# Optimization experiments

Hardware: AMD Instinct MI355X
Metric: run time of the kernel (lower is better)

Reference implementation:

```python
import jax, jax.numpy as jnp
import numpy as np

N_NODES = 50000
N_EDGES = 1600000
IN_DIM = 128
HIDDEN = 16
HEADS = 8
OUT_DIM = 64


def setup_inputs() -> dict:
    key = jax.random.key(0)
    k1, k2, k3, k4, k5 = jax.random.split(key, 5)
    h = jax.random.normal(k1, (N_NODES, IN_DIM), dtype=jnp.float32)
    W1 = jax.random.normal(k2, (IN_DIM, HEADS * HIDDEN), dtype=jnp.float32) * (IN_DIM ** -0.5)
    W2 = jax.random.normal(k3, (HEADS * HIDDEN, OUT_DIM), dtype=jnp.float32) * ((HEADS * HIDDEN) ** -0.5)
    src = jax.random.randint(k4, (N_EDGES,), 0, N_NODES, dtype=jnp.int32)
    dst = jax.random.randint(k5, (N_EDGES,), 0, N_NODES, dtype=jnp.int32)
    return {"h": h, "W1": W1, "W2": W2, "src": src, "dst": dst}


def dot_gat_conv(h, W, src, dst, num_heads, out_feats):
    # Project and split heads: [N, H, D]
    feat = (h @ W).reshape(-1, num_heads, out_feats)
    fs = feat[src]                       # [E, H, D] gather
    fd = feat[dst]                       # [E, H, D] gather
    scale = jnp.asarray(out_feats, feat.dtype) ** -0.5
    e = jnp.einsum('ehd,ehd->eh', fs, fd) * scale  # [E, H] scaled dot score
    # Edge softmax over incoming edges of each destination node
    m = jax.ops.segment_max(e, dst, num_segments=N_NODES)   # [N, H]
    m = jnp.where(jnp.isfinite(m), m, jnp.zeros_like(m))    # isolated nodes
    ex = jnp.exp(e - m[dst])                                 # [E, H]
    denom = jax.ops.segment_sum(ex, dst, num_segments=N_NODES)  # [N, H]
    a = ex / jnp.maximum(denom[dst], jnp.asarray(1e-9, ex.dtype))  # [E, H]
    # Weighted scatter-sum aggregation: [N, H, D]
    return jax.ops.segment_sum(a[:, :, None] * fs, dst, num_segments=N_NODES)


def reference(h, W1, W2, src, dst):
    h1 = dot_gat_conv(h, W1, src, dst, HEADS, HIDDEN)  # [N, H, hidden]
    h1 = jax.nn.elu(h1).reshape(N_NODES, HEADS * HIDDEN)  # flatten(1)
    # Dropout: eval-mode identity
    h2 = dot_gat_conv(h1, W2, src, dst, 1, OUT_DIM)  # [N, 1, out]
    return h2.mean(axis=1)  # [N, out]
```

## Files before the change

kernel.cpp:

```cpp
#include <hip/hip_runtime.h>
#include <hip/hip_bf16.h>

#define N_NODES 50000
#define N_EDGES 1600000
#define NBUCK 98
#define EPB 4096
#define NB_A ((N_EDGES + EPB - 1) / EPB)

typedef short bf16x8 __attribute__((ext_vector_type(8)));
typedef float f32x4  __attribute__((ext_vector_type(4)));

__device__ __forceinline__ float bf16_raw_to_f32(unsigned short u) {
    return __uint_as_float(((unsigned)u) << 16);
}
__device__ __forceinline__ unsigned short f32_to_bf16_raw(float v) {
    unsigned u = __float_as_uint(v);
    return (unsigned short)((u + 0x7fffu + ((u >> 16) & 1u)) >> 16);
}
__device__ __forceinline__ float load_elem(const void* p, size_t i, int f) {
    if (f) return ((const float*)p)[i];
    return bf16_raw_to_f32(((const unsigned short*)p)[i]);
}
__device__ __forceinline__ void unpack8(uint4 u, float* f) {
    f[0] = __uint_as_float(u.x << 16);
    f[1] = __uint_as_float(u.x & 0xffff0000u);
    f[2] = __uint_as_float(u.y << 16);
    f[3] = __uint_as_float(u.y & 0xffff0000u);
    f[4] = __uint_as_float(u.z << 16);
    f[5] = __uint_as_float(u.z & 0xffff0000u);
    f[6] = __uint_as_float(u.w << 16);
    f[7] = __uint_as_float(u.w & 0xffff0000u);
}

__device__ __forceinline__ void osm_upd(float sc, float& m, float& l,
                                        float* a, const float* fv) {
    float d  = sc - m;
    float t  = __expf(-fabsf(d));
    bool  up = d > 0.f;
    float sf = up ? t : 1.f;
    float w  = up ? 1.f : t;
    if (up) m = sc;
#pragma unroll
    for (int j = 0; j < 8; ++j) a[j] = fmaf(a[j], sf, w * fv[j]);
    l = fmaf(l, sf, w);
}

__global__ void detect_dtype_kernel(const unsigned short* __restrict__ w1raw,
                                    int* __restrict__ flag, int* __restrict__ bcnt) {
    __shared__ float red[256];
    if (threadIdx.x < NBUCK) bcnt[threadIdx.x] = 0;
    float mx = 0.f;
    for (int i = threadIdx.x * 2; i < 16384; i += 512) {
        float v = fabsf(bf16_raw_to_f32(w1raw[i]));
        if (!isnan(v)) mx = fmaxf(mx, v);
    }
    red[threadIdx.x] = mx;
    __syncthreads();
    for (int s = 128; s > 0; s >>= 1) {
        if (threadIdx.x < s) red[threadIdx.x] = fmaxf(red[threadIdx.x], red[threadIdx.x + s]);
        __syncthreads();
    }
    if (threadIdx.x == 0) flag[0] = (red[0] > 1e4f) ? 1 : 0;
}

#define WPAD 136
__global__ void prep_kernel(const void* __restrict__ W1, const void* __restrict__ W2,
                            unsigned short* __restrict__ W1T,
                            unsigned short* __restrict__ W2T,
                            const int* __restrict__ flag) {
    const int f = *flag;
    int bid = blockIdx.x, tid = threadIdx.x;
    if (bid < 8) {
        int n = bid * 16 + (tid & 15);
        int kb = (tid >> 4) * 8;
        for (int j = 0; j < 8; ++j)
            W1T[n * WPAD + kb + j] = f32_to_bf16_raw(load_elem(W1, (size_t)(kb + j) * 128 + n, f));
    } else {
        int n = (bid - 8) * 16 + (tid & 15);
        int kb = (tid >> 4) * 8;
        for (int j = 0; j < 8; ++j)
            W2T[n * WPAD + kb + j] = f32_to_bf16_raw(load_elem(W2, (size_t)(kb + j) * 64 + n, f));
    }
}

__global__ void bucket_count_kernel(const int* __restrict__ dst,
                                    int* __restrict__ bcnt, int E) {
    __shared__ int hist[NBUCK];
    int t = threadIdx.x;
    if (t < NBUCK) hist[t] = 0;
    __syncthreads();
    int e0 = blockIdx.x * EPB;
    for (int k = 0; k < 16; ++k) {
        int e = e0 + k * 256 + t;
        if (e < E) atomicAdd(&hist[dst[e] >> 9], 1);
    }
    __syncthreads();
    if (t < NBUCK && hist[t]) atomicAdd(&bcnt[t], hist[t]);
}

__global__ void bucket_scan_kernel(const int* __restrict__ bcnt,
                                   int* __restrict__ bbase, int* __restrict__ bcur) {
    __shared__ int tmp[128];
    int t = threadIdx.x;
    int v = (t < NBUCK) ? bcnt[t] : 0;
    tmp[t] = v;
    __syncthreads();
    for (int off = 1; off < 128; off <<= 1) {
        int x = (t >= off) ? tmp[t - off] : 0;
        __syncthreads();
        tmp[t] += x;
        __syncthreads();
    }
    if (t < NBUCK) { int ex = tmp[t] - v; bbase[t] = ex; bcur[t] = ex; }
    if (t == NBUCK - 1) bbase[NBUCK] = tmp[t];
}

__global__ void binA_kernel(const int* __restrict__ src, const int* __restrict__ dst,
                            int* __restrict__ bcur, unsigned* __restrict__ inter, int E) {
    __shared__ int hist[NBUCK], gbase[NBUCK], cur[NBUCK];
    int t = threadIdx.x;
    if (t < NBUCK) hist[t] = 0;
    __syncthreads();
    int e0 = blockIdx.x * EPB;
    for (int k = 0; k < 16; ++k) {
        int e = e0 + k * 256 + t;
        if (e < E) atomicAdd(&hist[dst[e] >> 9], 1);
    }
    __syncthreads();
    if (t < NBUCK) {
        int hv = hist[t];
        gbase[t] = hv ? atomicAdd(&bcur[t], hv) : 0;
        cur[t] = 0;
    }
    __syncthreads();
    for (int k = 0; k < 16; ++k) {
        int e = e0 + k * 256 + t;
        if (e < E) {
            int d = dst[e];
            int b = d >> 9;
            int off = atomicAdd(&cur[b], 1);
            inter[gbase[b] + off] = (unsigned)src[e] | ((unsigned)(d & 511) << 16);
        }
    }
}

__global__ void binB_kernel(const unsigned* __restrict__ inter,
                            const int* __restrict__ bbase,
                            int* __restrict__ csr_src, int* __restrict__ start,
                            int N, int E) {
    int b = blockIdx.x;
    int node0 = b << 9;
    int lo = bbase[b], hi = bbase[b + 1];
    __shared__ int hist[512];
    __shared__ int t2[256];
    int t = threadIdx.x;
    hist[t] = 0; hist[t + 256] = 0;
    __syncthreads();
    for (int e = lo + t; e < hi; e += 256) atomicAdd(&hist[inter[e] >> 16], 1);
    __syncthreads();
    int s0 = hist[2 * t], s1 = hist[2 * t + 1];
    t2[t] = s0 + s1;
    __syncthreads();
    for (int off = 1; off < 256; off <<= 1) {
        int x = (t >= off) ? t2[t - off] : 0;
        __syncthreads();
        t2[t] += x;
        __syncthreads();
    }
    int base = (t == 0) ? 0 : t2[t - 1];
    hist[2 * t] = base;
    hist[2 * t + 1] = base + s0;
    __syncthreads();
    int nodeCnt = min(512, N - node0);
    for (int i = t; i < nodeCnt; i += 256) start[node0 + i] = lo + hist[i];
    if (b == NBUCK - 1 && t == 0) start[N] = E;
    __syncthreads();
    for (int e = lo + t; e < hi; e += 256) {
        unsigned u = inter[e];
        int slot = lo + atomicAdd(&hist[u >> 16], 1);
        csr_src[slot] = (int)(u & 0xffffu);
    }
}

__global__ void gemm1_mfma_kernel(const void* __restrict__ h,
                                  const unsigned short* __restrict__ W1T,
                                  unsigned short* __restrict__ feat1, int N,
                                  const int* __restrict__ flag) {
    const int f = *flag;
    int lane = threadIdx.x & 63;
    int rbase = blockIdx.x * 64 + (threadIdx.x >> 6) * 16;
    int arow = rbase + (lane & 15);
    int arowc = min(arow, N - 1);
    int kb0 = (lane >> 4) * 8;

    f32x4 acc[8];
#pragma unroll
    for (int t = 0; t < 8; ++t) acc[t] = (f32x4){0.f, 0.f, 0.f, 0.f};

#pragma unroll
    for (int ks = 0; ks < 4; ++ks) {
        int kb = ks * 32 + kb0;
        bf16x8 afrag;
        if (f == 0) {
            afrag = *(const bf16x8*)((const unsigned short*)h + (size_t)arowc * 128 + kb);
        } else {
            const float* hp = (const float*)h + (size_t)arowc * 128 + kb;
#pragma unroll
            for (int j = 0; j < 8; ++j) afrag[j] = (short)f32_to_bf16_raw(hp[j]);
        }
#pragma unroll
        for (int t = 0; t < 8; ++t) {
            int n = t * 16 + (lane & 15);
            bf16x8 bfrag = *(const bf16x8*)(W1T + n * WPAD + kb);
            acc[t] = __builtin_amdgcn_mfma_f32_16x16x32_bf16(afrag, bfrag, acc[t], 0, 0, 0);
        }
    }
    int orow0 = rbase + (lane >> 4) * 4;
    int col = lane & 15;
#pragma unroll
    for (int t = 0; t < 8; ++t)
#pragma unroll
        for (int r = 0; r < 4; ++r) {
            int row = orow0 + r;
            if (row < N)
                feat1[(size_t)row * 128 + t * 16 + col] = f32_to_bf16_raw(acc[t][r]);
        }
}

__global__ void gemm2_mfma_kernel(const unsigned short* __restrict__ agg1e,
                                  const unsigned short* __restrict__ W2T,
                                  unsigned short* __restrict__ feat2, int N) {
    int lane = threadIdx.x & 63;
    int rbase = blockIdx.x * 64 + (threadIdx.x >> 6) * 16;
    int arow = rbase + (lane & 15);
    int arowc = min(arow, N - 1);
    int kb0 = (lane >> 4) * 8;

    f32x4 acc[4];
#pragma unroll
    for (int t = 0; t < 4; ++t) acc[t] = (f32x4){0.f, 0.f, 0.f, 0.f};

#pragma unroll
    for (int ks = 0; ks < 4; ++ks) {
        int kb = ks * 32 + kb0;
        bf16x8 afrag = *(const bf16x8*)(agg1e + (size_t)arowc * 128 + kb);
#pragma unroll
        for (int t = 0; t < 4; ++t) {
            int n = t * 16 + (lane & 15);
            bf16x8 bfrag = *(const bf16x8*)(W2T + n * WPAD + kb);
            acc[t] = __builtin_amdgcn_mfma_f32_16x16x32_bf16(afrag, bfrag, acc[t], 0, 0, 0);
        }
    }
    int orow0 = rbase + (lane >> 4) * 4;
    int col = lane & 15;
#pragma unroll
    for (int t = 0; t < 4; ++t)
#pragma unroll
        for (int r = 0; r < 4; ++r) {
            int row = orow0 + r;
            if (row < N)
                feat2[(size_t)row * 64 + t * 16 + col] = f32_to_bf16_raw(acc[t][r]);
        }
}

__global__ void gat1_kernel(const unsigned short* __restrict__ feat1,
                            const int* __restrict__ csr_src,
                            const int* __restrict__ start,
                            unsigned short* __restrict__ agg1e, int N) {
    int wave = blockIdx.x * 4 + (threadIdx.x >> 6);
    if (wave >= N) return;
    int lane = threadIdx.x & 63;
    int grp = lane >> 4, gl = lane & 15;
    const char* fb = (const char*)feat1;
    unsigned loff = (unsigned)gl << 4;
    float fd[8];
    unpack8(*(const uint4*)(fb + (((unsigned)wave << 8) + loff)), fd);

    float m = -__builtin_inff(), l = 0.f, a[8];
#pragma unroll
    for (int j = 0; j < 8; ++j) a[j] = 0.f;

    int e0 = start[wave], e1 = start[wave + 1];
    int base = e0;
    for (; base + 8 <= e1; base += 8) {
        int s0 = csr_src[base + grp];
        int s1 = csr_src[base + 4 + grp];
        uint4 u0 = *(const uint4*)(fb + (((unsigned)s0 << 8) + loff));
        uint4 u1 = *(const uint4*)(fb + (((unsigned)s1 << 8) + loff));
        float f0[8], f1[8];
        unpack8(u0, f0); unpack8(u1, f1);
        float p0 = 0.f, p1 = 0.f;
#pragma unroll
        for (int j = 0; j < 8; ++j) { p0 += fd[j] * f0[j]; p1 += fd[j] * f1[j]; }
        p0 += __shfl_xor(p0, 1);
        p1 += __shfl_xor(p1, 1);
        osm_upd(p0 * 0.25f, m, l, a, f0);
        osm_upd(p1 * 0.25f, m, l, a, f1);
    }
    for (; base < e1; base += 4) {
        int ed = base + grp;
        bool act = ed < e1;
        int s = act ? csr_src[ed] : 0;
        uint4 u = *(const uint4*)(fb + (((unsigned)s << 8) + loff));
        float fv[8]; unpack8(u, fv);
        float p = 0.f;
#pragma unroll
        for (int j = 0; j < 8; ++j) p += fd[j] * fv[j];
        p += __shfl_xor(p, 1);
        if (act) osm_upd(p * 0.25f, m, l, a, fv);
    }
#pragma unroll
    for (int off = 16; off <= 32; off <<= 1) {
        float mo = __shfl_xor(m, off), lo = __shfl_xor(l, off);
        float bfr[8];
#pragma unroll
        for (int j = 0; j < 8; ++j) bfr[j] = __shfl_xor(a[j], off);
        float mn = fmaxf(m, mo);
        float sA = (m == mn) ? 1.f : __expf(m - mn);
        float sB = (mo == mn) ? 1.f : __expf(mo - mn);
#pragma unroll
        for (int j = 0; j < 8; ++j) a[j] = a[j] * sA + bfr[j] * sB;
        l = l * sA + lo * sB; m = mn;
    }
    if (grp == 0) {
        float rcp = 1.f / fmaxf(l, 1e-9f);
        float v[8];
#pragma unroll
        for (int j = 0; j < 8; ++j) {
            float x = a[j] * rcp;
            v[j] = (x > 0.f) ? x : expm1f(x);
        }
        uint4 pk;
        pk.x = (unsigned)f32_to_bf16_raw(v[0]) | ((unsigned)f32_to_bf16_raw(v[1]) << 16);
        pk.y = (unsigned)f32_to_bf16_raw(v[2]) | ((unsigned)f32_to_bf16_raw(v[3]) << 16);
        pk.z = (unsigned)f32_to_bf16_raw(v[4]) | ((unsigned)f32_to_bf16_raw(v[5]) << 16);
        pk.w = (unsigned)f32_to_bf16_raw(v[6]) | ((unsigned)f32_to_bf16_raw(v[7]) << 16);
        *(uint4*)(agg1e + (size_t)wave * 128 + gl * 8) = pk;
    }
}

__global__ void gat2_kernel(const unsigned short* __restrict__ feat2,
                            const int* __restrict__ csr_src,
                            const int* __restrict__ start,
                            void* __restrict__ out, int N,
                            const int* __restrict__ flag) {
    int wave = blockIdx.x * 4 + (threadIdx.x >> 6);
    if (wave >= N) return;
    int lane = threadIdx.x & 63;
    int grp = lane >> 3, gl = lane & 7;
    const int f = *flag;
    const char* fb = (const char*)feat2;
    unsigned loff = (unsigned)gl << 4;
    float fd[8];
    unpack8(*(const uint4*)(fb + (((unsigned)wave << 7) + loff)), fd);

    float m = -__builtin_inff(), l = 0.f, a[8];
#pragma unroll
    for (int j = 0; j < 8; ++j) a[j] = 0.f;

    int e0 = start[wave], e1 = start[wave + 1];
    int base = e0;
    for (; base + 16 <= e1; base += 16) {
        int s0 = csr_src[base + grp];
        int s1 = csr_src[base + 8 + grp];
        uint4 u0 = *(const uint4*)(fb + (((unsigned)s0 << 7) + loff));
        uint4 u1 = *(const uint4*)(fb + (((unsigned)s1 << 7) + loff));
        float f0[8], f1[8];
        unpack8(u0, f0); unpack8(u1, f1);
        float p0 = 0.f, p1 = 0.f;
#pragma unroll
        for (int j = 0; j < 8; ++j) { p0 += fd[j] * f0[j]; p1 += fd[j] * f1[j]; }
        p0 += __shfl_xor(p0, 1); p1 += __shfl_xor(p1, 1);
        p0 += __shfl_xor(p0, 2); p1 += __shfl_xor(p1, 2);
        p0 += __shfl_xor(p0, 4); p1 += __shfl_xor(p1, 4);
        osm_upd(p0 * 0.125f, m, l, a, f0);
        osm_upd(p1 * 0.125f, m, l, a, f1);
    }
    for (; base < e1; base += 8) {
        int ed = base + grp;
        bool act = ed < e1;
        int s = act ? csr_src[ed] : 0;
        uint4 u = *(const uint4*)(fb + (((unsigned)s << 7) + loff));
        float fv[8]; unpack8(u, fv);
        float p = 0.f;
#pragma unroll
        for (int j = 0; j < 8; ++j) p += fd[j] * fv[j];
        p += __shfl_xor(p, 1);
        p += __shfl_xor(p, 2);
        p += __shfl_xor(p, 4);
        if (act) osm_upd(p * 0.125f, m, l, a, fv);
    }
#pragma unroll
    for (int off = 8; off <= 32; off <<= 1) {
        float mo = __shfl_xor(m, off), lo = __shfl_xor(l, off);
        float bfr[8];
#pragma unroll
        for (int j = 0; j < 8; ++j) bfr[j] = __shfl_xor(a[j], off);
        float mn = fmaxf(m, mo);
        float sA = (m == mn) ? 1.f : __expf(m - mn);
        float sB = (mo == mn) ? 1.f : __expf(mo - mn);
#pragma unroll
        for (int j = 0; j < 8; ++j) a[j] = a[j] * sA + bfr[j] * sB;
        l = l * sA + lo * sB; m = mn;
    }
    if (grp == 0) {
        float rcp = 1.f / fmaxf(l, 1e-9f);
        float v[8];
#pragma unroll
        for (int j = 0; j < 8; ++j) v[j] = a[j] * rcp;
        if (f) {
            float* op = (float*)out + (size_t)wave * 64 + gl * 8;
            *(float4*)(op)     = (float4){v[0], v[1], v[2], v[3]};
            *(float4*)(op + 4) = (float4){v[4], v[5], v[6], v[7]};
        } else {
            uint4 pk;
            pk.x = (unsigned)f32_to_bf16_raw(v[0]) | ((unsigned)f32_to_bf16_raw(v[1]) << 16);
            pk.y = (unsigned)f32_to_bf16_raw(v[2]) | ((unsigned)f32_to_bf16_raw(v[3]) << 16);
            pk.z = (unsigned)f32_to_bf16_raw(v[4]) | ((unsigned)f32_to_bf16_raw(v[5]) << 16);
            pk.w = (unsigned)f32_to_bf16_raw(v[6]) | ((unsigned)f32_to_bf16_raw(v[7]) << 16);
            *(uint4*)((unsigned short*)out + (size_t)wave * 64 + gl * 8) = pk;
        }
    }
}

extern "C" void kernel_launch(void* const* d_in, const int* in_sizes, int n_in,
                              void* d_out, int out_size, void* d_ws, size_t ws_size,
                              hipStream_t stream) {
    const void* h  = d_in[0];
    const void* W1 = d_in[1];
    const void* W2 = d_in[2];
    const int* src = (const int*)d_in[3];
    const int* dst = (const int*)d_in[4];

    float* ws = (float*)d_ws;
    unsigned short* feat1 = (unsigned short*)ws;
    unsigned short* agg1e = (unsigned short*)(ws + 3200000);
    unsigned short* feat2 = (unsigned short*)ws;
    unsigned* inter       = (unsigned*)(ws + 6400000);
    int*   csr_src        = (int*)(ws + 9600000);
    int*   start          = (int*)(ws + 11200000);
    int*   flag           = (int*)(ws + 11330000);
    int*   bcnt           = (int*)(ws + 11331000);
    int*   bbase          = (int*)(ws + 11332000);
    int*   bcur           = (int*)(ws + 11333000);
    unsigned short* W1T   = (unsigned short*)(ws + 11340000);
    unsigned short* W2T   = (unsigned short*)(ws + 11350000);

    detect_dtype_kernel<<<1, 256, 0, stream>>>((const unsigned short*)W1, flag, bcnt);
    prep_kernel<<<12, 256, 0, stream>>>(W1, W2, W1T, W2T, flag);

    bucket_count_kernel<<<NB_A, 256, 0, stream>>>(dst, bcnt, N_EDGES);
    bucket_scan_kernel<<<1, 128, 0, stream>>>(bcnt, bbase, bcur);
    binA_kernel<<<NB_A, 256, 0, stream>>>(src, dst, bcur, inter, N_EDGES);
    binB_kernel<<<NBUCK, 256, 0, stream>>>(inter, bbase, csr_src, start, N_NODES, N_EDGES);

    gemm1_mfma_kernel<<<(N_NODES + 63) / 64, 256, 0, stream>>>(h, W1T, feat1, N_NODES, flag);
    gat1_kernel<<<(N_NODES + 3) / 4, 256, 0, stream>>>(feat1, csr_src, start, agg1e, N_NODES);
    gemm2_mfma_kernel<<<(N_NODES + 63) / 64, 256, 0, stream>>>(agg1e, W2T, feat2, N_NODES);
    gat2_kernel<<<(N_NODES + 3) / 4, 256, 0, stream>>>(feat2, csr_src, start, d_out, N_NODES, flag);
}
```

Before: 295.3 us.

## Use Cauchy-Schwarz softmax shift and fixed-capacity buckets to drop extra passes

New measurement: 303.6 us. 1.03x slower.

```diff
diff --git a/kernel.cpp b/kernel.cpp
--- a/kernel.cpp
+++ b/kernel.cpp
@@ -6,6 +6,7 @@
 #define NBUCK 98
 #define EPB 4096
 #define NB_A ((N_EDGES + EPB - 1) / EPB)
+#define CAP 20480
 
 typedef short bf16x8 __attribute__((ext_vector_type(8)));
 typedef float f32x4  __attribute__((ext_vector_type(4)));
@@ -32,35 +33,27 @@
     f[7] = __uint_as_float(u.w & 0xffff0000u);
 }
 
-__device__ __forceinline__ void osm_upd(float sc, float& m, float& l,
-                                        float* a, const float* fv) {
-    float d  = sc - m;
-    float t  = __expf(-fabsf(d));
-    bool  up = d > 0.f;
-    float sf = up ? t : 1.f;
-    float w  = up ? 1.f : t;
-    if (up) m = sc;
-#pragma unroll
-    for (int j = 0; j < 8; ++j) a[j] = fmaf(a[j], sf, w * fv[j]);
-    l = fmaf(l, sf, w);
-}
-
 __global__ void detect_dtype_kernel(const unsigned short* __restrict__ w1raw,
-                                    int* __restrict__ flag, int* __restrict__ bcnt) {
+                                    int* __restrict__ flag, int* __restrict__ bcur,
+                                    unsigned* __restrict__ n1max,
+                                    unsigned* __restrict__ n2max) {
     __shared__ float red[256];
-    if (threadIdx.x < NBUCK) bcnt[threadIdx.x] = 0;
+    int t = threadIdx.x;
+    if (t < NBUCK) bcur[t] = t * CAP;
+    if (t < 8) n1max[t] = 0u;
+    if (t == 8) n2max[0] = 0u;
     float mx = 0.f;
-    for (int i = threadIdx.x * 2; i < 16384; i += 512) {
+    for (int i = t * 2; i < 16384; i += 512) {
         float v = fabsf(bf16_raw_to_f32(w1raw[i]));
         if (!isnan(v)) mx = fmaxf(mx, v);
     }
-    red[threadIdx.x] = mx;
+    red[t] = mx;
     __syncthreads();
     for (int s = 128; s > 0; s >>= 1) {
-        if (threadIdx.x < s) red[threadIdx.x] = fmaxf(red[threadIdx.x], red[threadIdx.x + s]);
+        if (t < s) red[t] = fmaxf(red[t], red[t + s]);
         __syncthreads();
     }
-    if (threadIdx.x == 0) flag[0] = (red[0] > 1e4f) ? 1 : 0;
+    if (t == 0) flag[0] = (red[0] > 1e4f) ? 1 : 0;
 }
 
 #define WPAD 136
@@ -83,38 +76,6 @@
     }
 }
 
-__global__ void bucket_count_kernel(const int* __restrict__ dst,
-                                    int* __restrict__ bcnt, int E) {
-    __shared__ int hist[NBUCK];
-    int t = threadIdx.x;
-    if (t < NBUCK) hist[t] = 0;
-    __syncthreads();
-    int e0 = blockIdx.x * EPB;
-    for (int k = 0; k < 16; ++k) {
-        int e = e0 + k * 256 + t;
-        if (e < E) atomicAdd(&hist[dst[e] >> 9], 1);
-    }
-    __syncthreads();
-    if (t < NBUCK && hist[t]) atomicAdd(&bcnt[t], hist[t]);
-}
-
-__global__ void bucket_scan_kernel(const int* __restrict__ bcnt,
-                                   int* __restrict__ bbase, int* __restrict__ bcur) {
-    __shared__ int tmp[128];
-    int t = threadIdx.x;
-    int v = (t < NBUCK) ? bcnt[t] : 0;
-    tmp[t] = v;
-    __syncthreads();
-    for (int off = 1; off < 128; off <<= 1) {
-        int x = (t >= off) ? tmp[t - off] : 0;
-        __syncthreads();
-        tmp[t] += x;
-        __syncthreads();
-    }
-    if (t < NBUCK) { int ex = tmp[t] - v; bbase[t] = ex; bcur[t] = ex; }
-    if (t == NBUCK - 1) bbase[NBUCK] = tmp[t];
-}
-
 __global__ void binA_kernel(const int* __restrict__ src, const int* __restrict__ dst,
                             int* __restrict__ bcur, unsigned* __restrict__ inter, int E) {
     __shared__ int hist[NBUCK], gbase[NBUCK], cur[NBUCK];
@@ -144,19 +105,37 @@
     }
 }
 
+__global__ void bucket_scan_kernel(const int* __restrict__ bcur, int* __restrict__ bbase) {
+    __shared__ int tmp[128];
+    int t = threadIdx.x;
+    int v = (t < NBUCK) ? (bcur[t] - t * CAP) : 0;
+    tmp[t] = v;
+    __syncthreads();
+    for (int off = 1; off < 128; off <<= 1) {
+        int x = (t >= off) ? tmp[t - off] : 0;
+        __syncthreads();
+        tmp[t] += x;
+        __syncthreads();
+    }
+    if (t < NBUCK) bbase[t] = tmp[t] - v;
+    if (t == NBUCK - 1) bbase[NBUCK] = tmp[t];
+}
+
 __global__ void binB_kernel(const unsigned* __restrict__ inter,
                             const int* __restrict__ bbase,
                             int* __restrict__ csr_src, int* __restrict__ start,
                             int N, int E) {
     int b = blockIdx.x;
     int node0 = b << 9;
-    int lo = bbase[b], hi = bbase[b + 1];
+    int inbase = b * CAP;
+    int obase = bbase[b];
+    int cnt = bbase[b + 1] - obase;
     __shared__ int hist[512];
     __shared__ int t2[256];
     int t = threadIdx.x;
     hist[t] = 0; hist[t + 256] = 0;
     __syncthreads();
-    for (int e = lo + t; e < hi; e += 256) atomicAdd(&hist[inter[e] >> 16], 1);
+    for (int e = t; e < cnt; e += 256) atomicAdd(&hist[inter[inbase + e] >> 16], 1);
     __syncthreads();
     int s0 = hist[2 * t], s1 = hist[2 * t + 1];
     t2[t] = s0 + s1;
@@ -172,12 +151,12 @@
     hist[2 * t + 1] = base + s0;
     __syncthreads();
     int nodeCnt = min(512, N - node0);
-    for (int i = t; i < nodeCnt; i += 256) start[node0 + i] = lo + hist[i];
+    for (int i = t; i < nodeCnt; i += 256) start[node0 + i] = obase + hist[i];
     if (b == NBUCK - 1 && t == 0) start[N] = E;
     __syncthreads();
-    for (int e = lo + t; e < hi; e += 256) {
-        unsigned u = inter[e];
-        int slot = lo + atomicAdd(&hist[u >> 16], 1);
+    for (int e = t; e < cnt; e += 256) {
+        unsigned u = inter[inbase + e];
+        int slot = obase + atomicAdd(&hist[u >> 16], 1);
         csr_src[slot] = (int)(u & 0xffffu);
     }
 }
@@ -263,20 +242,73 @@
         }
 }
 
+__global__ void norms1_kernel(const unsigned short* __restrict__ feat1,
+                              float* __restrict__ n1, unsigned* __restrict__ n1max,
+                              int N) {
+    __shared__ unsigned bmax[8];
+    if (threadIdx.x < 8) bmax[threadIdx.x] = 0u;
+    __syncthreads();
+    int gid = blockIdx.x * 256 + threadIdx.x;
+    if (gid < N * 8) {
+        int v = gid >> 3, hd = gid & 7;
+        const uint4* p = (const uint4*)(feat1 + (size_t)v * 128 + hd * 16);
+        float f[8]; float s = 0.f;
+        unpack8(p[0], f);
+#pragma unroll
+        for (int j = 0; j < 8; ++j) s += f[j] * f[j];
+        unpack8(p[1], f);
+#pragma unroll
+        for (int j = 0; j < 8; ++j) s += f[j] * f[j];
+        float n = sqrtf(s);
+        n1[gid] = n;
+        atomicMax(&bmax[hd], __float_as_uint(n));
+    }
+    __syncthreads();
+    if (threadIdx.x < 8 && bmax[threadIdx.x]) atomicMax(&n1max[threadIdx.x], bmax[threadIdx.x]);
+}
+
+__global__ void norms2_kernel(const unsigned short* __restrict__ feat2,
+                              float* __restrict__ n2, unsigned* __restrict__ n2max,
+                              int N) {
+    __shared__ unsigned bmax;
+    if (threadIdx.x == 0) bmax = 0u;
+    __syncthreads();
+    int v = blockIdx.x * 256 + threadIdx.x;
+    if (v < N) {
+        const uint4* p = (const uint4*)(feat2 + (size_t)v * 64);
+        float s = 0.f;
+#pragma unroll
+        for (int q = 0; q < 8; ++q) {
+            float f[8]; unpack8(p[q], f);
+#pragma unroll
+            for (int j = 0; j < 8; ++j) s += f[j] * f[j];
+        }
+        float n = sqrtf(s);
+        n2[v] = n;
+        atomicMax(&bmax, __float_as_uint(n));
+    }
+    __syncthreads();
+    if (threadIdx.x == 0 && bmax) atomicMax(n2max, bmax);
+}
+
 __global__ void gat1_kernel(const unsigned short* __restrict__ feat1,
                             const int* __restrict__ csr_src,
                             const int* __restrict__ start,
+                            const float* __restrict__ n1,
+                            const float* __restrict__ n1max,
                             unsigned short* __restrict__ agg1e, int N) {
     int wave = blockIdx.x * 4 + (threadIdx.x >> 6);
     if (wave >= N) return;
     int lane = threadIdx.x & 63;
     int grp = lane >> 4, gl = lane & 15;
+    int hd = gl >> 1;
     const char* fb = (const char*)feat1;
     unsigned loff = (unsigned)gl << 4;
     float fd[8];
     unpack8(*(const uint4*)(fb + (((unsigned)wave << 8) + loff)), fd);
-
-    float m = -__builtin_inff(), l = 0.f, a[8];
+    float M = 0.25f * n1[wave * 8 + hd] * n1max[hd];
+
+    float l = 0.f, a[8];
 #pragma unroll
     for (int j = 0; j < 8; ++j) a[j] = 0.f;
 
@@ -294,8 +326,13 @@
         for (int j = 0; j < 8; ++j) { p0 += fd[j] * f0[j]; p1 += fd[j] * f1[j]; }
         p0 += __shfl_xor(p0, 1);
         p1 += __shfl_xor(p1, 1);
-        osm_upd(p0 * 0.25f, m, l, a, f0);
-        osm_upd(p1 * 0.25f, m, l, a, f1);
+        float w0 = __expf(fmaf(p0, 0.25f, -M));
+        float w1 = __expf(fmaf(p1, 0.25f, -M));
+#pragma unroll
+        for (int j = 0; j < 8; ++j) a[j] = fmaf(w0, f0[j], a[j]);
+#pragma unroll
+        for (int j = 0; j < 8; ++j) a[j] = fmaf(w1, f1[j], a[j]);
+        l += w0 + w1;
     }
     for (; base < e1; base += 4) {
         int ed = base + grp;
@@ -307,20 +344,18 @@
 #pragma unroll
         for (int j = 0; j < 8; ++j) p += fd[j] * fv[j];
         p += __shfl_xor(p, 1);
-        if (act) osm_upd(p * 0.25f, m, l, a, fv);
+        if (act) {
+            float w = __expf(fmaf(p, 0.25f, -M));
+#pragma unroll
+            for (int j = 0; j < 8; ++j) a[j] = fmaf(w, fv[j], a[j]);
+            l += w;
+        }
     }
 #pragma unroll
     for (int off = 16; off <= 32; off <<= 1) {
-        float mo = __shfl_xor(m, off), lo = __shfl_xor(l, off);
-        float bfr[8];
-#pragma unroll
-        for (int j = 0; j < 8; ++j) bfr[j] = __shfl_xor(a[j], off);
-        float mn = fmaxf(m, mo);
-        float sA = (m == mn) ? 1.f : __expf(m - mn);
-        float sB = (mo == mn) ? 1.f : __expf(mo - mn);
-#pragma unroll
-        for (int j = 0; j < 8; ++j) a[j] = a[j] * sA + bfr[j] * sB;
-        l = l * sA + lo * sB; m = mn;
+#pragma unroll
+        for (int j = 0; j < 8; ++j) a[j] += __shfl_xor(a[j], off);
+        l += __shfl_xor(l, off);
     }
     if (grp == 0) {
         float rcp = 1.f / fmaxf(l, 1e-9f);
@@ -342,6 +377,8 @@
 __global__ void gat2_kernel(const unsigned short* __restrict__ feat2,
                             const int* __restrict__ csr_src,
                             const int* __restrict__ start,
+                            const float* __restrict__ n2,
+                            const float* __restrict__ n2max,
                             void* __restrict__ out, int N,
                             const int* __restrict__ flag) {
     int wave = blockIdx.x * 4 + (threadIdx.x >> 6);
@@ -353,8 +390,9 @@
     unsigned loff = (unsigned)gl << 4;
     float fd[8];
     unpack8(*(const uint4*)(fb + (((unsigned)wave << 7) + loff)), fd);
-
-    float m = -__builtin_inff(), l = 0.f, a[8];
+    float M = 0.125f * n2[wave] * n2max[0];
+
+    float l = 0.f, a[8];
 #pragma unroll
     for (int j = 0; j < 8; ++j) a[j] = 0.f;
 
@@ -373,8 +411,13 @@
         p0 += __shfl_xor(p0, 1); p1 += __shfl_xor(p1, 1);
         p0 += __shfl_xor(p0, 2); p1 += __shfl_xor(p1, 2);
         p0 += __shfl_xor(p0, 4); p1 += __shfl_xor(p1, 4);
-        osm_upd(p0 * 0.125f, m, l, a, f0);
-        osm_upd(p1 * 0.125f, m, l, a, f1);
+        float w0 = __expf(fmaf(p0, 0.125f, -M));
+        float w1 = __expf(fmaf(p1, 0.125f, -M));
+#pragma unroll
+        for (int j = 0; j < 8; ++j) a[j] = fmaf(w0, f0[j], a[j]);
+#pragma unroll
+        for (int j = 0; j < 8; ++j) a[j] = fmaf(w1, f1[j], a[j]);
+        l += w0 + w1;
     }
     for (; base < e1; base += 8) {
         int ed = base + grp;
@@ -388,20 +431,18 @@
         p += __shfl_xor(p, 1);
         p += __shfl_xor(p, 2);
         p += __shfl_xor(p, 4);
-        if (act) osm_upd(p * 0.125f, m, l, a, fv);
+        if (act) {
+            float w = __expf(fmaf(p, 0.125f, -M));
+#pragma unroll
+            for (int j = 0; j < 8; ++j) a[j] = fmaf(w, fv[j], a[j]);
+            l += w;
+        }
     }
 #pragma unroll
     for (int off = 8; off <= 32; off <<= 1) {
-        float mo = __shfl_xor(m, off), lo = __shfl_xor(l, off);
-        float bfr[8];
-#pragma unroll
-        for (int j = 0; j < 8; ++j) bfr[j] = __shfl_xor(a[j], off);
-        float mn = fmaxf(m, mo);
-        float sA = (m == mn) ? 1.f : __expf(m - mn);
-        float sB = (mo == mn) ? 1.f : __expf(mo - mn);
-#pragma unroll
-        for (int j = 0; j < 8; ++j) a[j] = a[j] * sA + bfr[j] * sB;
-        l = l * sA + lo * sB; m = mn;
+#pragma unroll
+        for (int j = 0; j < 8; ++j) a[j] += __shfl_xor(a[j], off);
+        l += __shfl_xor(l, off);
     }
     if (grp == 0) {
         float rcp = 1.f / fmaxf(l, 1e-9f);
@@ -437,25 +478,29 @@
     unsigned short* agg1e = (unsigned short*)(ws + 3200000);
     unsigned short* feat2 = (unsigned short*)ws;
     unsigned* inter       = (unsigned*)(ws + 6400000);
+    float* n1             = ws + 8500000;
+    float* n2             = ws + 8900000;
     int*   csr_src        = (int*)(ws + 9600000);
     int*   start          = (int*)(ws + 11200000);
     int*   flag           = (int*)(ws + 11330000);
-    int*   bcnt           = (int*)(ws + 11331000);
     int*   bbase          = (int*)(ws + 11332000);
     int*   bcur           = (int*)(ws + 11333000);
+    unsigned* n1max       = (unsigned*)(ws + 11334000);
+    unsigned* n2max       = (unsigned*)(ws + 11334016);
     unsigned short* W1T   = (unsigned short*)(ws + 11340000);
     unsigned short* W2T   = (unsigned short*)(ws + 11350000);
 
-    detect_dtype_kernel<<<1, 256, 0, stream>>>((const unsigned short*)W1, flag, bcnt);
+    detect_dtype_kernel<<<1, 256, 0, stream>>>((const unsigned short*)W1, flag, bcur, n1max, n2max);
     prep_kernel<<<12, 256, 0, stream>>>(W1, W2, W1T, W2T, flag);
 
-    bucket_count_kernel<<<NB_A, 256, 0, stream>>>(dst, bcnt, N_EDGES);
-    bucket_scan_kernel<<<1, 128, 0, stream>>>(bcnt, bbase, bcur);
     binA_kernel<<<NB_A, 256, 0, stream>>>(src, dst, bcur, inter, N_EDGES);
+    bucket_scan_kernel<<<1, 128, 0, stream>>>(bcur, bbase);
     binB_kernel<<<NBUCK, 256, 0, stream>>>(inter, bbase, csr_src, start, N_NODES, N_EDGES);
 
     gemm1_mfma_kernel<<<(N_NODES + 63) / 64, 256, 0, stream>>>(h, W1T, feat1, N_NODES, flag);
-    gat1_kernel<<<(N_NODES + 3) / 4, 256, 0, stream>>>(feat1, csr_src, start, agg1e, N_NODES);
+    norms1_kernel<<<(N_NODES * 8 + 255) / 256, 256, 0, stream>>>(feat1, n1, n1max, N_NODES);
+    gat1_kernel<<<(N_NODES + 3) / 4, 256, 0, stream>>>(feat1, csr_src, start, n1, (const float*)n1max, agg1e, N_NODES);
     gemm2_mfma_kernel<<<(N_NODES + 63) / 64, 256, 0, stream>>>(agg1e, W2T, feat2, N_NODES);
-    gat2_kernel<<<(N_NODES + 3) / 4, 256, 0, stream>>>(feat2, csr_src, start, d_out, N_NODES, flag);
-}
+    norms2_kernel<<<(N_NODES + 255) / 256, 256, 0, stream>>>(feat2, n2, n2max, N_NODES);
+    gat2_kernel<<<(N_NODES + 3) / 4, 256, 0, stream>>>(feat2, csr_src, start, n2, (const float*)n2max, d_out, N_NODES, flag);
+}
```
